# Performance work log

Hardware: AMD Instinct MI355X
Metric: run time of the kernel (lower is better)

The kernel has to match this reference:

```python
import jax, jax.numpy as jnp
import numpy as np

P_SIZES = (1, 2, 4)
O_SIZE = 32
EPS = 1e-5


def bilin_matrix(S, O):
    """Interpolation matrix (O, S) for torch UpsamplingBilinear2d (align_corners=True)."""
    if S == 1:
        return jnp.ones((O, 1), dtype=jnp.float32)
    pos = jnp.arange(O, dtype=jnp.float32) * ((S - 1) / (O - 1))
    lo = jnp.clip(jnp.floor(pos).astype(jnp.int32), 0, S - 2)
    frac = pos - lo.astype(jnp.float32)
    rows = jnp.arange(O)
    M = jnp.zeros((O, S), dtype=jnp.float32)
    M = M.at[rows, lo].add(1.0 - frac).at[rows, lo + 1].add(frac)
    return M


def setup_inputs() -> dict:
    key = jax.random.key(0)
    ks = jax.random.split(key, 12)
    n, C, H = 16, 512, 32
    c4 = C // 4      # 128, value/pyramid channels
    qk = c4 // 8     # 16, query/key channels inside SAE
    s = 0.05
    return {
        "x": jax.random.normal(ks[0], (n, C, H, H), jnp.float32),
        "rce_w": jax.random.normal(ks[1], (3, c4, C), jnp.float32) * s,   # 1x1 conv per pyramid scale
        "rce_b": jax.random.normal(ks[2], (3, c4), jnp.float32) * s,
        "q_w": jax.random.normal(ks[3], (qk, c4), jnp.float32) * s,       # SAE query 1x1 conv
        "q_b": jax.random.normal(ks[4], (qk,), jnp.float32) * s,
        "k_w": jax.random.normal(ks[5], (qk, c4), jnp.float32) * s,       # SAE key 1x1 conv
        "k_b": jax.random.normal(ks[6], (qk,), jnp.float32) * s,
        "value_w": jax.random.normal(ks[7], (c4, C), jnp.float32) * s,    # value 1x1 conv
        "value_b": jax.random.normal(ks[8], (c4,), jnp.float32) * s,
        "fusion_w": jax.random.normal(ks[9], (C, 3 * c4, 3, 3), jnp.float32) * s,  # 3x3 conv, no bias
        "bn_scale": 1.0 + jax.random.normal(ks[10], (C,), jnp.float32) * s,
        "bn_bias": jax.random.normal(ks[11], (C,), jnp.float32) * s,
        "gamma": jnp.asarray(0.5, jnp.float32),
    }


def reference(x, rce_w, rce_b, q_w, q_b, k_w, k_b, value_w, value_b,
              fusion_w, bn_scale, bn_bias, gamma):
    n, C, H, W = x.shape
    c4 = C // 4
    L = H * W

    # value projection: 1x1 conv then flatten -> (n, c4, L)
    proj_value = (jnp.einsum('oc,nchw->nohw', value_w, x)
                  + value_b[None, :, None, None]).reshape(n, c4, L)

    outs = []
    for i, sz in enumerate(P_SIZES):
        # AdaptiveAvgPool2d((sz, sz)) with divisible input -> exact uniform pooling
        pooled = x.reshape(n, C, sz, H // sz, sz, W // sz).mean(axis=(3, 5))
        # 1x1 conv C -> c4
        feat = jnp.einsum('oc,ncij->noij', rce_w[i], pooled) + rce_b[i][None, :, None, None]
        # bilinear upsample (align_corners=True) to (O_SIZE, O_SIZE)
        M = bilin_matrix(sz, O_SIZE)
        up = jnp.einsum('oi,pj,ncij->ncop', M, M, feat)  # (n, c4, H, W)
        # SAE: query/key 1x1 convs, flatten, bmm + softmax
        q = (jnp.einsum('oc,nchw->nohw', q_w, up) + q_b[None, :, None, None]).reshape(n, -1, L)
        k = (jnp.einsum('oc,nchw->nohw', k_w, up) + k_b[None, :, None, None]).reshape(n, -1, L)
        energy = jnp.einsum('ncl,ncm->nlm', q, k)        # (n, L, L)
        attn = jax.nn.softmax(energy, axis=-1)
        # temp = bmm(value, attn^T): temp[c,m] = sum_l value[c,l] * attn[m,l]
        outs.append(jnp.einsum('ncl,nml->ncm', proj_value, attn).reshape(n, c4, H, W))

    cat = jnp.concatenate(outs, axis=1)                  # (n, 3*c4, H, W)
    y = jax.lax.conv_general_dilated(
        cat, fusion_w, window_strides=(1, 1), padding=((1, 1), (1, 1)),
        dimension_numbers=('NCHW', 'OIHW', 'NCHW'))
    # BatchNorm2d in training mode (default): batch statistics over (N, H, W)
    mean = y.mean(axis=(0, 2, 3))
    var = y.var(axis=(0, 2, 3))
    y = (y - mean[None, :, None, None]) * (bn_scale / jnp.sqrt(var + EPS))[None, :, None, None] \
        + bn_bias[None, :, None, None]
    y = jax.nn.relu(y)
    return gamma * y + x
```

## Files before the change

kernel.cpp:

```cpp
#include <hip/hip_runtime.h>
#include <hip/hip_fp16.h>
#include <math.h>

#define OFF_COR   0u
#define OFF_PVH   2097152u
#define OFF_Y     3145728u
#define OFF_CATP  11534336u
#define OFF_QH    15085568u
#define OFF_KH    15347712u
#define OFF_POOL  16134144u
#define OFF_FEAT  16297984u
#define OFF_AW    16338944u
#define OFF_MEANS 17223680u
#define OFF_STAT  17225728u
#define OFF_VWH   17226752u

typedef __bf16 bf16x8 __attribute__((ext_vector_type(8)));
typedef _Float16 f16x8 __attribute__((ext_vector_type(8)));
typedef _Float16 f16x4 __attribute__((ext_vector_type(4)));
typedef float f32x4 __attribute__((ext_vector_type(4)));

__device__ __forceinline__ unsigned short f2bf(float f) {
  unsigned int u = __float_as_uint(f);
  unsigned int r = u + 0x7fff + ((u >> 16) & 1);
  return (unsigned short)(r >> 16);
}

__device__ __forceinline__ unsigned short f2h(float f) {
  union { _Float16 h; unsigned short u; } cv;
  cv.h = (_Float16)f;
  return cv.u;
}

__device__ __forceinline__ void gload_lds16(const void* g, void* l) {
  __builtin_amdgcn_global_load_lds(
      (const __attribute__((address_space(1))) unsigned int*)g,
      (__attribute__((address_space(3))) unsigned int*)l, 16, 0, 0);
}

__global__ __launch_bounds__(256) void pool_kernel(const float* __restrict__ x,
                                                   float* __restrict__ pool) {
  int b = blockIdx.x;
  int t = threadIdx.x;
  const float4* xp = (const float4*)(x + (size_t)b * 1024);
  float4 v = xp[t];
  float s4 = v.x + v.y + v.z + v.w;
  __shared__ float sm[256];
  __shared__ float p4s[16];
  sm[t] = s4;
  __syncthreads();
  if (t < 16) {
    int br = t >> 2, bc = t & 3;
    float s = 0.f;
#pragma unroll
    for (int rr = 0; rr < 8; ++rr) {
      int base = br * 64 + rr * 8 + bc * 2;
      s += sm[base] + sm[base + 1];
    }
    s *= (1.f / 64.f);
    p4s[t] = s;
    pool[(size_t)b * 20 + t] = s;
  }
  __syncthreads();
  if (t < 4) {
    int i2 = t >> 1, j2 = t & 1;
    float s = (p4s[(2*i2)*4 + 2*j2]     + p4s[(2*i2)*4 + 2*j2 + 1] +
               p4s[(2*i2+1)*4 + 2*j2]   + p4s[(2*i2+1)*4 + 2*j2 + 1]) * 0.25f;
    pool[(size_t)b * 20 + 16 + t] = s;
  }
}

__global__ __launch_bounds__(64) void feat_kernel(const float* __restrict__ pool,
                                                  const float* __restrict__ rce_w,
                                                  const float* __restrict__ rce_b,
                                                  float* __restrict__ feat) {
  int o = blockIdx.x, n = blockIdx.y, t = threadIdx.x;
  float part[20];
#pragma unroll
  for (int j = 0; j < 20; ++j) part[j] = 0.f;
  for (int c = t; c < 512; c += 64) {
    const float* pl = pool + ((size_t)n * 512 + c) * 20;
    float w2 = rce_w[(size_t)(128 + o) * 512 + c];
    float w4 = rce_w[(size_t)(256 + o) * 512 + c];
#pragma unroll
    for (int j = 0; j < 4; ++j)  part[j]     += w2 * pl[16 + j];
#pragma unroll
    for (int j = 0; j < 16; ++j) part[4 + j] += w4 * pl[j];
  }
  __shared__ float red[64][20];
#pragma unroll
  for (int j = 0; j < 20; ++j) red[t][j] = part[j];
  __syncthreads();
  if (t < 20) {
    float s = 0.f;
    for (int i = 0; i < 64; ++i) s += red[i][t];
    s += (t < 4) ? rce_b[128 + o] : rce_b[256 + o];
    feat[((size_t)n * 128 + o) * 20 + t] = s;
  }
}

__global__ __launch_bounds__(256) void qk2_kernel(const float* __restrict__ feat,
                                                  const float* __restrict__ q_w,
                                                  const float* __restrict__ q_b,
                                                  const float* __restrict__ k_w,
                                                  const float* __restrict__ k_b,
                                                  unsigned short* __restrict__ qh,
                                                  unsigned short* __restrict__ kh) {
  int n = blockIdx.x, t = threadIdx.x;
  __shared__ float fL[128 * 20];
  __shared__ float GH[2][16][20];
  for (int idx = t; idx < 2560; idx += 256) fL[idx] = feat[(size_t)n * 2560 + idx];
  __syncthreads();
  for (int idx = t; idx < 640; idx += 256) {
    int which = idx / 320, rem = idx % 320, qc = rem / 20, j = rem % 20;
    const float* w = which ? k_w : q_w;
    float s = which ? k_b[qc] : q_b[qc];
    for (int c = 0; c < 128; ++c) s += w[qc * 128 + c] * fL[c * 20 + j];
    GH[which][qc][j] = s;
  }
  __syncthreads();
  for (int it = 0; it < 16; ++it) {
    int row = t + 256 * it;
    int l = row & 1023, which = (row >> 10) & 1, s = row >> 11;
    int ry = l >> 5, cx = l & 31;
    int t0, t1, t2, t3;
    float w0, w1, w2, w3;
    if (s == 0) {
      float a = ry * (1.0f / 31.0f), b = cx * (1.0f / 31.0f);
      t0 = 0; t1 = 1; t2 = 2; t3 = 3;
      w0 = (1.f - a) * (1.f - b); w1 = (1.f - a) * b;
      w2 = a * (1.f - b);         w3 = a * b;
    } else {
      float pr = ry * (3.0f / 31.0f);
      int lr = (int)pr; if (lr > 2) lr = 2;
      float fr = pr - (float)lr;
      float pc = cx * (3.0f / 31.0f);
      int lc = (int)pc; if (lc > 2) lc = 2;
      float fc = pc - (float)lc;
      int base = 4 + lr * 4 + lc;
      t0 = base; t1 = base + 1; t2 = base + 4; t3 = base + 5;
      w0 = (1.f - fr) * (1.f - fc); w1 = (1.f - fr) * fc;
      w2 = fr * (1.f - fc);         w3 = fr * fc;
    }
    float val[16];
#pragma unroll
    for (int qc = 0; qc < 16; ++qc) {
      const float* G = GH[which][qc];
      val[qc] = w0 * G[t0] + w1 * G[t1] + w2 * G[t2] + w3 * G[t3];
    }
    unsigned short* dst = (which ? kh : qh) + (((size_t)(s * 16 + n) * 1024 + l) * 16);
#pragma unroll
    for (int u = 0; u < 4; ++u)
      *(ushort4*)(dst + 4 * u) = make_ushort4(f2h(val[4*u]), f2h(val[4*u+1]),
                                              f2h(val[4*u+2]), f2h(val[4*u+3]));
  }
}

__global__ __launch_bounds__(256) void xcast_kernel(const float* __restrict__ x,
                                                    unsigned short* __restrict__ xT) {
  int lt = blockIdx.x, ct = blockIdx.y, n = blockIdx.z;
  int l0 = lt * 64, c0 = ct * 64, t = threadIdx.x;
  __shared__ float tile[64 * 65];
#pragma unroll
  for (int i = 0; i < 16; ++i) {
    int idx = t + 256 * i;
    int c = idx >> 6, l = idx & 63;
    tile[c * 65 + l] = x[((size_t)n * 512 + c0 + c) * 1024 + l0 + l];
  }
  __syncthreads();
#pragma unroll
  for (int i = 0; i < 16; ++i) {
    int idx = t + 256 * i;
    int l = idx >> 6, c = idx & 63;
    xT[((size_t)n * 1024 + l0 + l) * 512 + c0 + c] = f2h(tile[c * 65 + l]);
  }
}

__global__ __launch_bounds__(256) void vwcast_kernel(const float* __restrict__ vw,
                                                     unsigned short* __restrict__ vwh) {
  int i = blockIdx.x * 256 + threadIdx.x;
  vwh[i] = f2h(vw[i]);
}

__global__ __launch_bounds__(256) void pvmm2_kernel(const unsigned short* __restrict__ vwh,
                                                    const unsigned short* __restrict__ xT,
                                                    const float* __restrict__ vb,
                                                    unsigned short* __restrict__ pvh) {
  int l0 = blockIdx.x * 64;
  int n = blockIdx.y;
  int t = threadIdx.x, lane = t & 63, wv = t >> 6;
  int wm = (wv & 1) * 64, wn = (wv >> 1) * 32;

  __shared__ short Asm[128 * 32];
  __shared__ short Bsm[64 * 32];

  int ar0 = t >> 2,        aq0 = (t & 3) ^ ((ar0 >> 1) & 3);
  int idx1 = t + 256; int ar1 = idx1 >> 2, aq1 = (idx1 & 3) ^ ((ar1 >> 1) & 3);
  int br  = t >> 2,        bq  = (t & 3) ^ ((br >> 1) & 3);
  const unsigned short* Ab0 = vwh + (size_t)ar0 * 512 + aq0 * 8;
  const unsigned short* Ab1 = vwh + (size_t)ar1 * 512 + aq1 * 8;
  const unsigned short* Bb  = xT + ((size_t)n * 1024 + l0 + br) * 512 + bq * 8;
  char* ldsA = (char*)Asm;
  char* ldsB = (char*)Bsm;
  int wvoff = wv * 1024;
  int r15 = lane & 15, kg = lane >> 4;
  int kq = kg ^ ((r15 >> 1) & 3);

  f32x4 acc[4][2];
#pragma unroll
  for (int i = 0; i < 4; ++i)
#pragma unroll
    for (int j = 0; j < 2; ++j) acc[i][j] = (f32x4){0.f, 0.f, 0.f, 0.f};

  for (int k0 = 0; k0 < 512; k0 += 32) {
    __syncthreads();
    gload_lds16(Ab0 + k0, ldsA + wvoff);
    gload_lds16(Ab1 + k0, ldsA + 4096 + wvoff);
    gload_lds16(Bb + k0,  ldsB + wvoff);
    __syncthreads();
    f16x8 af[4], bfr[2];
#pragma unroll
    for (int mt2 = 0; mt2 < 4; ++mt2)
      af[mt2] = *(const f16x8*)&Asm[(wm + mt2 * 16 + r15) * 32 + kq * 8];
#pragma unroll
    for (int nt2 = 0; nt2 < 2; ++nt2)
      bfr[nt2] = *(const f16x8*)&Bsm[(wn + nt2 * 16 + r15) * 32 + kq * 8];
#pragma unroll
    for (int mt2 = 0; mt2 < 4; ++mt2)
#pragma unroll
      for (int nt2 = 0; nt2 < 2; ++nt2)
        acc[mt2][nt2] = __builtin_amdgcn_mfma_f32_16x16x32_f16(af[mt2], bfr[nt2], acc[mt2][nt2], 0, 0, 0);
  }

  int c_lo = wm + (lane >> 4) * 4;
  int l_lo = wn + (lane & 15);
#pragma unroll
  for (int mt2 = 0; mt2 < 4; ++mt2)
#pragma unroll
    for (int nt2 = 0; nt2 < 2; ++nt2) {
      int l = l0 + l_lo + nt2 * 16;
#pragma unroll
      for (int r = 0; r < 4; ++r) {
        int c = c_lo + mt2 * 16 + r;
        pvh[((size_t)n * 128 + c) * 1024 + l] = f2h(acc[mt2][nt2][r] + vb[c]);
      }
    }
}

__global__ __launch_bounds__(256) void mean_kernel(const unsigned short* __restrict__ pvh,
                                                   float* __restrict__ means) {
  int c = blockIdx.x, n = blockIdx.y, t = threadIdx.x;
  f16x4 v = ((const f16x4*)(pvh + ((size_t)n * 128 + c) * 1024))[t];
  float s = (float)v[0] + (float)v[1] + (float)v[2] + (float)v[3];
  for (int o = 32; o > 0; o >>= 1) s += __shfl_down(s, o);
  __shared__ float wsum[4];
  if ((t & 63) == 0) wsum[t >> 6] = s;
  __syncthreads();
  if (t == 0) means[n * 128 + c] = (wsum[0] + wsum[1] + wsum[2] + wsum[3]) * (1.f / 1024.f);
}

__global__ __launch_bounds__(64) void basecor_kernel(const float* __restrict__ means,
                                                     const float* __restrict__ fw,
                                                     float* __restrict__ cor) {
  int oc = blockIdx.x, n = blockIdx.y, t = threadIdx.x;
  float S[9];
#pragma unroll
  for (int j = 0; j < 9; ++j) S[j] = 0.f;
  for (int c = t; c < 128; c += 64) {
    float m = means[n * 128 + c];
    const float* wp = fw + (size_t)oc * 3456 + c * 9;
#pragma unroll
    for (int j = 0; j < 9; ++j) S[j] += m * wp[j];
  }
  __shared__ float red[64][9];
  __shared__ float Sf[9];
#pragma unroll
  for (int j = 0; j < 9; ++j) red[t][j] = S[j];
  __syncthreads();
  if (t < 9) {
    float s = 0.f;
    for (int i = 0; i < 64; ++i) s += red[i][t];
    Sf[t] = s;
  }
  __syncthreads();
  if (t < 9) {
    int a = t / 3, b = t % 3;
    float s = 0.f;
#pragma unroll
    for (int ky = 0; ky < 3; ++ky) {
      if ((a == 0 && ky == 0) || (a == 2 && ky == 2)) continue;
#pragma unroll
      for (int kx = 0; kx < 3; ++kx) {
        if ((b == 0 && kx == 0) || (b == 2 && kx == 2)) continue;
        s += Sf[ky * 3 + kx];
      }
    }
    cor[((size_t)n * 512 + oc) * 9 + t] = s;
  }
}

__global__ __launch_bounds__(128) void fillcat_kernel(unsigned short* __restrict__ catp) {
  int b = blockIdx.x;
  int n = b / 132, e = b % 132;
  int py, px;
  if (e < 34)       { py = 0;          px = e; }
  else if (e < 68)  { py = 33;         px = e - 34; }
  else if (e < 100) { py = e - 68 + 1; px = 0; }
  else              { py = e - 100 + 1; px = 33; }
  unsigned int* row = (unsigned int*)(catp + ((size_t)n * 1156 + py * 34 + px) * 256);
  row[threadIdx.x] = 0u;
}

__global__ __launch_bounds__(256) void wcast_kernel(const float* __restrict__ fw,
                                                    unsigned short* __restrict__ Aw) {
  int oc = blockIdx.x, t = threadIdx.x;
  for (int j = t; j < 2304; j += 256) {
    int seg = j >> 8, ic2 = j & 255;
    Aw[(size_t)oc * 2304 + j] = f2bf(fw[(size_t)oc * 3456 + (128 + ic2) * 9 + seg]);
  }
}

__global__ __launch_bounds__(256) void fattn_kernel(const unsigned short* __restrict__ qh,
                                                    const unsigned short* __restrict__ kh,
                                                    const unsigned short* __restrict__ pvh,
                                                    unsigned short* __restrict__ catp) {
  int m0 = blockIdx.x * 64;
  int n = blockIdx.y, sc = blockIdx.z;
  int t = threadIdx.x, lane = t & 63, wv = t >> 6;
  int wc = (wv >> 1) * 64;
  int wm2 = (wv & 1) * 32;
  int r15 = lane & 15, kg = lane >> 4;
  int kq = kg ^ ((r15 >> 1) & 3);

  const unsigned short* qb  = qh + ((size_t)(sc * 16 + n) * 1024 + m0 + wv * 16) * 16;
  const unsigned short* kb  = kh + ((size_t)(sc * 16 + n) * 1024) * 16;
  const unsigned short* pvb = pvh + (size_t)n * 128 * 1024;

  __shared__ short PVs[2 * 128 * 32];
  __shared__ _Float16 Us[64 * 72];
  __shared__ float rsum[64];

  f16x8 zf = {0, 0, 0, 0, 0, 0, 0, 0};
  f16x8 qa = (kg < 2) ? *(const f16x8*)(qb + r15 * 16 + kg * 8) : zf;

  int prow = t >> 2;
  int aq = (t & 3) ^ ((prow >> 1) & 3);
  const unsigned short* Pb0 = pvb + (size_t)prow * 1024 + aq * 8;
  const unsigned short* Pb1 = pvb + (size_t)(prow + 64) * 1024 + aq * 8;
  char* ldsPV = (char*)PVs;
  int wvoff = wv * 1024;

  f32x4 acc[4][2];
#pragma unroll
  for (int i = 0; i < 4; ++i)
#pragma unroll
    for (int j = 0; j < 2; ++j) acc[i][j] = (f32x4){0.f, 0.f, 0.f, 0.f};
  float rs[4] = {0.f, 0.f, 0.f, 0.f};

  for (int it = 0; it < 16; ++it) {
    int l0 = it * 64;
    __syncthreads();
    gload_lds16(Pb0 + l0,      ldsPV + wvoff);
    gload_lds16(Pb1 + l0,      ldsPV + 4096 + wvoff);
    gload_lds16(Pb0 + l0 + 32, ldsPV + 8192 + wvoff);
    gload_lds16(Pb1 + l0 + 32, ldsPV + 12288 + wvoff);

    f32x4 sacc[4];
#pragma unroll
    for (int lt = 0; lt < 4; ++lt) {
      f16x8 kbf = (kg < 2)
        ? *(const f16x8*)(kb + (size_t)(l0 + lt * 16 + r15) * 16 + kg * 8) : zf;
      sacc[lt] = __builtin_amdgcn_mfma_f32_16x16x32_f16(qa, kbf, (f32x4){0.f,0.f,0.f,0.f}, 0, 0, 0);
    }
#pragma unroll
    for (int lt = 0; lt < 4; ++lt)
#pragma unroll
      for (int r = 0; r < 4; ++r) {
        float e = __expf(sacc[lt][r]);
        Us[(wv * 16 + kg * 4 + r) * 72 + lt * 16 + r15] = (_Float16)e;
        rs[r] += e;
      }
    __syncthreads();

#pragma unroll
    for (int ks = 0; ks < 2; ++ks) {
      f16x8 bfr[2];
#pragma unroll
      for (int nt = 0; nt < 2; ++nt)
        bfr[nt] = *(const f16x8*)&Us[(wm2 + nt * 16 + r15) * 72 + ks * 32 + kg * 8];
#pragma unroll
      for (int ct = 0; ct < 4; ++ct) {
        f16x8 af = *(const f16x8*)&PVs[ks * 4096 + (wc + ct * 16 + r15) * 32 + kq * 8];
#pragma unroll
        for (int nt = 0; nt < 2; ++nt)
          acc[ct][nt] = __builtin_amdgcn_mfma_f32_16x16x32_f16(af, bfr[nt], acc[ct][nt], 0, 0, 0);
      }
    }
  }

#pragma unroll
  for (int r = 0; r < 4; ++r) {
    rs[r] += __shfl_xor(rs[r], 1);
    rs[r] += __shfl_xor(rs[r], 2);
    rs[r] += __shfl_xor(rs[r], 4);
    rs[r] += __shfl_xor(rs[r], 8);
  }
  if (r15 == 0) {
#pragma unroll
    for (int r = 0; r < 4; ++r) rsum[wv * 16 + kg * 4 + r] = rs[r];
  }
  __syncthreads();

#pragma unroll
  for (int nt = 0; nt < 2; ++nt) {
    float inv = 1.f / rsum[wm2 + nt * 16 + r15];
    int pix = m0 + wm2 + nt * 16 + r15;
    unsigned short* ob = catp + ((size_t)n * 1156 + ((pix >> 5) + 1) * 34 + (pix & 31) + 1) * 256
                       + sc * 128 + wc + kg * 4;
#pragma unroll
    for (int ct = 0; ct < 4; ++ct) {
      ushort4 o = make_ushort4(f2bf(acc[ct][nt][0] * inv), f2bf(acc[ct][nt][1] * inv),
                               f2bf(acc[ct][nt][2] * inv), f2bf(acc[ct][nt][3] * inv));
      *(ushort4*)(ob + ct * 16) = o;
    }
  }
}

__device__ __forceinline__ void conv_stage(const unsigned short* __restrict__ Aw,
                                           const unsigned short* __restrict__ catp,
                                           size_t abase0, size_t abase1,
                                           size_t bbase0, size_t bbase1,
                                           int s, char* la, char* lb, int wvoff) {
  int seg = s >> 2;
  size_t akk  = (size_t)s * 64;
  size_t boff = (size_t)((seg / 3) * 34 + (seg % 3)) * 256 + (size_t)(s & 3) * 64;
  gload_lds16(Aw + abase0 + akk,          la + wvoff);
  gload_lds16(Aw + abase1 + akk,          la + 4096 + wvoff);
  gload_lds16(Aw + abase0 + akk + 32,     la + 8192 + wvoff);
  gload_lds16(Aw + abase1 + akk + 32,     la + 12288 + wvoff);
  gload_lds16(catp + bbase0 + boff,       lb + wvoff);
  gload_lds16(catp + bbase1 + boff,       lb + 4096 + wvoff);
  gload_lds16(catp + bbase0 + boff + 32,  lb + 8192 + wvoff);
  gload_lds16(catp + bbase1 + boff + 32,  lb + 12288 + wvoff);
}

__device__ __forceinline__ void conv_comp(const short* As_, const short* Bs_,
                                          int wm, int wn, int r15, int kq,
                                          f32x4 acc[4][4]) {
  bf16x8 af[4], bf[4];
#pragma unroll
  for (int mt = 0; mt < 4; ++mt)
    af[mt] = *(const bf16x8*)&As_[(wm + mt * 16 + r15) * 32 + kq * 8];
#pragma unroll
  for (int nt = 0; nt < 4; ++nt)
    bf[nt] = *(const bf16x8*)&Bs_[(wn + nt * 16 + r15) * 32 + kq * 8];
#pragma unroll
  for (int mt = 0; mt < 4; ++mt)
#pragma unroll
    for (int nt = 0; nt < 4; ++nt)
      acc[mt][nt] = __builtin_amdgcn_mfma_f32_16x16x32_bf16(af[mt], bf[nt], acc[mt][nt], 0, 0, 0);
}

__global__ __launch_bounds__(256) void convmm_kernel(const unsigned short* __restrict__ Aw,
                                                     const unsigned short* __restrict__ catp,
                                                     const float* __restrict__ cor,
                                                     float* __restrict__ y) {
  int ntile = blockIdx.x;
  int n = ntile >> 3, y0 = (ntile & 7) * 4;
  int m0 = blockIdx.y * 128;
  int t = threadIdx.x;
  int lane = t & 63, wv = t >> 6;
  int wm = (wv & 1) * 64, wn = (wv >> 1) * 64;

  __shared__ short Asm[2 * 2 * 128 * 32];
  __shared__ short Bsm[2 * 2 * 128 * 32];

  int idx0 = t, idx1 = t + 256;
  int ar0 = idx0 >> 2, aq0 = (idx0 & 3) ^ ((ar0 >> 1) & 3);
  int ar1 = idx1 >> 2, aq1 = (idx1 & 3) ^ ((ar1 >> 1) & 3);
  size_t abase0 = (size_t)(m0 + ar0) * 2304 + aq0 * 8;
  size_t abase1 = (size_t)(m0 + ar1) * 2304 + aq1 * 8;
  size_t bbase0 = ((size_t)n * 1156 + (size_t)(y0 + (ar0 >> 5)) * 34 + (ar0 & 31)) * 256 + aq0 * 8;
  size_t bbase1 = ((size_t)n * 1156 + (size_t)(y0 + (ar1 >> 5)) * 34 + (ar1 & 31)) * 256 + aq1 * 8;
  char* ldsA = (char*)Asm;
  char* ldsB = (char*)Bsm;
  int wvoff = wv * 1024;

  int r15 = lane & 15, kg = lane >> 4;
  int kq = kg ^ ((r15 >> 1) & 3);

  f32x4 acc[4][4];
#pragma unroll
  for (int i = 0; i < 4; ++i)
#pragma unroll
    for (int j = 0; j < 4; ++j) acc[i][j] = (f32x4){0.f, 0.f, 0.f, 0.f};

  conv_stage(Aw, catp, abase0, abase1, bbase0, bbase1, 0, ldsA, ldsB, wvoff);
  __syncthreads();

#pragma unroll 2
  for (int s = 0; s < 36; ++s) {
    char* la = ldsA + (s & 1) * 16384;
    char* lb = ldsB + (s & 1) * 16384;
    if (s < 35)
      conv_stage(Aw, catp, abase0, abase1, bbase0, bbase1, s + 1,
                 ldsA + ((s + 1) & 1) * 16384, ldsB + ((s + 1) & 1) * 16384, wvoff);
    conv_comp((const short*)la,          (const short*)lb,          wm, wn, r15, kq, acc);
    conv_comp((const short*)(la + 8192), (const short*)(lb + 8192), wm, wn, r15, kq, acc);
    __syncthreads();
  }

  int pixbase = (ntile & 7) * 128 + wn + (lane & 15);
  int ocbase = m0 + wm + (lane >> 4) * 4;
#pragma unroll
  for (int mt = 0; mt < 4; ++mt)
#pragma unroll
    for (int nt = 0; nt < 4; ++nt) {
      int oc = ocbase + mt * 16;
      int pix = pixbase + nt * 16;
      int py = pix >> 5, px = pix & 31;
      int yc = (py == 0) ? 0 : ((py == 31) ? 2 : 1);
      int xc = (px == 0) ? 0 : ((px == 31) ? 2 : 1);
      const float* cp = cor + ((size_t)n * 512 + oc) * 9 + yc * 3 + xc;
      float* yp = y + ((size_t)n * 512 + oc) * 1024 + pix;
#pragma unroll
      for (int r = 0; r < 4; ++r) yp[(size_t)r * 1024] = acc[mt][nt][r] + cp[(size_t)r * 9];
    }
}

__global__ __launch_bounds__(256) void bnstat_kernel(const float* __restrict__ y,
                                                     const float* __restrict__ bn_scale,
                                                     const float* __restrict__ bn_bias,
                                                     float* __restrict__ stats) {
  int oc = blockIdx.x, t = threadIdx.x;
  float s = 0.f, ss = 0.f;
  for (int n = 0; n < 16; ++n) {
    float4 v = ((const float4*)(y + ((size_t)n * 512 + oc) * 1024))[t];
    s  += v.x + v.y + v.z + v.w;
    ss += v.x * v.x + v.y * v.y + v.z * v.z + v.w * v.w;
  }
  for (int o = 32; o > 0; o >>= 1) {
    s  += __shfl_down(s, o);
    ss += __shfl_down(ss, o);
  }
  __shared__ float rs[4], rss[4];
  if ((t & 63) == 0) { rs[t >> 6] = s; rss[t >> 6] = ss; }
  __syncthreads();
  if (t == 0) {
    float S = rs[0] + rs[1] + rs[2] + rs[3];
    float SS = rss[0] + rss[1] + rss[2] + rss[3];
    float mean = S * (1.f / 16384.f);
    float var = SS * (1.f / 16384.f) - mean * mean;
    float se = bn_scale[oc] / sqrtf(var + 1e-5f);
    stats[oc * 2] = se;
    stats[oc * 2 + 1] = bn_bias[oc] - mean * se;
  }
}

__global__ __launch_bounds__(256) void final_kernel(const float* __restrict__ y,
                                                    const float* __restrict__ x,
                                                    const float* __restrict__ stats,
                                                    const float* __restrict__ gamma,
                                                    float* __restrict__ outp) {
  int b = blockIdx.x;
  int c = b & 511;
  int t = threadIdx.x;
  float se = stats[c * 2], sh = stats[c * 2 + 1], g = gamma[0];
  float4 yv = ((const float4*)(y + (size_t)b * 1024))[t];
  float4 xv = ((const float4*)(x + (size_t)b * 1024))[t];
  float4 o;
  o.x = g * fmaxf(yv.x * se + sh, 0.f) + xv.x;
  o.y = g * fmaxf(yv.y * se + sh, 0.f) + xv.y;
  o.z = g * fmaxf(yv.z * se + sh, 0.f) + xv.z;
  o.w = g * fmaxf(yv.w * se + sh, 0.f) + xv.w;
  ((float4*)(outp + (size_t)b * 1024))[t] = o;
}

extern "C" void kernel_launch(void* const* d_in, const int* in_sizes, int n_in,
                              void* d_out, int out_size, void* d_ws, size_t ws_size,
                              hipStream_t stream) {
  const float* x        = (const float*)d_in[0];
  const float* rce_w    = (const float*)d_in[1];
  const float* rce_b    = (const float*)d_in[2];
  const float* q_w      = (const float*)d_in[3];
  const float* q_b      = (const float*)d_in[4];
  const float* k_w      = (const float*)d_in[5];
  const float* k_b      = (const float*)d_in[6];
  const float* value_w  = (const float*)d_in[7];
  const float* value_b  = (const float*)d_in[8];
  const float* fw       = (const float*)d_in[9];
  const float* bn_scale = (const float*)d_in[10];
  const float* bn_bias  = (const float*)d_in[11];
  const float* gamma    = (const float*)d_in[12];

  float* ws    = (float*)d_ws;
  float* cor   = ws + OFF_COR;
  unsigned short* pvh = (unsigned short*)(ws + OFF_PVH);
  float* ybuf  = ws + OFF_Y;
  unsigned short* xTbuf = (unsigned short*)(ws + OFF_Y);
  unsigned short* catp = (unsigned short*)(ws + OFF_CATP);
  unsigned short* qh   = (unsigned short*)(ws + OFF_QH);
  unsigned short* kh   = (unsigned short*)(ws + OFF_KH);
  float* pool  = ws + OFF_POOL;
  float* feat  = ws + OFF_FEAT;
  unsigned short* Aw = (unsigned short*)(ws + OFF_AW);
  float* means = ws + OFF_MEANS;
  float* stats = ws + OFF_STAT;
  unsigned short* vwh = (unsigned short*)(ws + OFF_VWH);
  float* outp  = (float*)d_out;

  hipLaunchKernelGGL(pool_kernel,    dim3(8192),       dim3(256), 0, stream, x, pool);
  hipLaunchKernelGGL(feat_kernel,    dim3(128, 16),    dim3(64),  0, stream, pool, rce_w, rce_b, feat);
  hipLaunchKernelGGL(qk2_kernel,     dim3(16),         dim3(256), 0, stream, feat, q_w, q_b, k_w, k_b, qh, kh);
  hipLaunchKernelGGL(xcast_kernel,   dim3(16, 8, 16),  dim3(256), 0, stream, x, xTbuf);
  hipLaunchKernelGGL(vwcast_kernel,  dim3(256),        dim3(256), 0, stream, value_w, vwh);
  hipLaunchKernelGGL(pvmm2_kernel,   dim3(16, 16),     dim3(256), 0, stream, vwh, xTbuf, value_b, pvh);
  hipLaunchKernelGGL(mean_kernel,    dim3(128, 16),    dim3(256), 0, stream, pvh, means);
  hipLaunchKernelGGL(basecor_kernel, dim3(512, 16),    dim3(64),  0, stream, means, fw, cor);
  hipLaunchKernelGGL(fillcat_kernel, dim3(2112),       dim3(128), 0, stream, catp);
  hipLaunchKernelGGL(wcast_kernel,   dim3(512),        dim3(256), 0, stream, fw, Aw);
  hipLaunchKernelGGL(fattn_kernel,   dim3(16, 16, 2),  dim3(256), 0, stream, qh, kh, pvh, catp);
  hipLaunchKernelGGL(convmm_kernel,  dim3(128, 4),     dim3(256), 0, stream, Aw, catp, cor, ybuf);
  hipLaunchKernelGGL(bnstat_kernel,  dim3(512),        dim3(256), 0, stream, ybuf, bn_scale, bn_bias, stats);
  hipLaunchKernelGGL(final_kernel,   dim3(8192),       dim3(256), 0, stream, ybuf, x, stats, gamma, outp);
}
```

Before: 259.7 us.

## Double-buffer PV tiles in attention kernel and split qk2 across more blocks

The fused attention kernel now keeps two LDS buffers for the projected-value tiles. It prefetches the next tile while the current one is consumed, and replaces the __syncthreads calls with explicit waitcnt and s_barrier so the global-to-LDS load overlaps the QK/exp and PV MFMA work. Separately, qk2_kernel is launched on a 16x8 grid, with each block handling 2 of the 16 row iterations instead of all of them, which raises parallelism for that small kernel. The cost is double the LDS for the PV buffers, which may lower occupancy, plus a redundant recompute of the per-batch G matrix in every y-block.

```diff
diff --git a/kernel.cpp b/kernel.cpp
--- a/kernel.cpp
+++ b/kernel.cpp
@@ -119,7 +119,7 @@
     GH[which][qc][j] = s;
   }
   __syncthreads();
-  for (int it = 0; it < 16; ++it) {
+  for (int it = blockIdx.y * 2; it < blockIdx.y * 2 + 2; ++it) {
     int row = t + 256 * it;
     int l = row & 1023, which = (row >> 10) & 1, s = row >> 11;
     int ry = l >> 5, cx = l & 31;
@@ -336,7 +336,7 @@
   const unsigned short* kb  = kh + ((size_t)(sc * 16 + n) * 1024) * 16;
   const unsigned short* pvb = pvh + (size_t)n * 128 * 1024;
 
-  __shared__ short PVs[2 * 128 * 32];
+  __shared__ short PVs[2 * 2 * 128 * 32];
   __shared__ _Float16 Us[64 * 72];
   __shared__ float rsum[64];
 
@@ -357,21 +357,30 @@
     for (int j = 0; j < 2; ++j) acc[i][j] = (f32x4){0.f, 0.f, 0.f, 0.f};
   float rs[4] = {0.f, 0.f, 0.f, 0.f};
 
+  gload_lds16(Pb0,      ldsPV + wvoff);
+  gload_lds16(Pb1,      ldsPV + 4096 + wvoff);
+  gload_lds16(Pb0 + 32, ldsPV + 8192 + wvoff);
+  gload_lds16(Pb1 + 32, ldsPV + 12288 + wvoff);
+
   for (int it = 0; it < 16; ++it) {
+    int cur = it & 1;
     int l0 = it * 64;
-    __syncthreads();
-    gload_lds16(Pb0 + l0,      ldsPV + wvoff);
-    gload_lds16(Pb1 + l0,      ldsPV + 4096 + wvoff);
-    gload_lds16(Pb0 + l0 + 32, ldsPV + 8192 + wvoff);
-    gload_lds16(Pb1 + l0 + 32, ldsPV + 12288 + wvoff);
-
+    f16x8 kbf[4];
+#pragma unroll
+    for (int lt = 0; lt < 4; ++lt)
+      kbf[lt] = (kg < 2)
+        ? *(const f16x8*)(kb + (size_t)(l0 + lt * 16 + r15) * 16 + kg * 8) : zf;
+    if (it < 15) {
+      char* dst = ldsPV + (cur ^ 1) * 16384 + wvoff;
+      gload_lds16(Pb0 + l0 + 64, dst);
+      gload_lds16(Pb1 + l0 + 64, dst + 4096);
+      gload_lds16(Pb0 + l0 + 96, dst + 8192);
+      gload_lds16(Pb1 + l0 + 96, dst + 12288);
+    }
     f32x4 sacc[4];
 #pragma unroll
-    for (int lt = 0; lt < 4; ++lt) {
-      f16x8 kbf = (kg < 2)
-        ? *(const f16x8*)(kb + (size_t)(l0 + lt * 16 + r15) * 16 + kg * 8) : zf;
-      sacc[lt] = __builtin_amdgcn_mfma_f32_16x16x32_f16(qa, kbf, (f32x4){0.f,0.f,0.f,0.f}, 0, 0, 0);
-    }
+    for (int lt = 0; lt < 4; ++lt)
+      sacc[lt] = __builtin_amdgcn_mfma_f32_16x16x32_f16(qa, kbf[lt], (f32x4){0.f,0.f,0.f,0.f}, 0, 0, 0);
 #pragma unroll
     for (int lt = 0; lt < 4; ++lt)
 #pragma unroll
@@ -380,8 +389,9 @@
         Us[(wv * 16 + kg * 4 + r) * 72 + lt * 16 + r15] = (_Float16)e;
         rs[r] += e;
       }
-    __syncthreads();
-
+    asm volatile("s_waitcnt vmcnt(4) lgkmcnt(0)" ::: "memory");
+    __builtin_amdgcn_s_barrier();
+    __builtin_amdgcn_sched_barrier(0);
 #pragma unroll
     for (int ks = 0; ks < 2; ++ks) {
       f16x8 bfr[2];
@@ -390,12 +400,15 @@
         bfr[nt] = *(const f16x8*)&Us[(wm2 + nt * 16 + r15) * 72 + ks * 32 + kg * 8];
 #pragma unroll
       for (int ct = 0; ct < 4; ++ct) {
-        f16x8 af = *(const f16x8*)&PVs[ks * 4096 + (wc + ct * 16 + r15) * 32 + kq * 8];
+        f16x8 af = *(const f16x8*)&PVs[cur * 8192 + ks * 4096 + (wc + ct * 16 + r15) * 32 + kq * 8];
 #pragma unroll
         for (int nt = 0; nt < 2; ++nt)
           acc[ct][nt] = __builtin_amdgcn_mfma_f32_16x16x32_f16(af, bfr[nt], acc[ct][nt], 0, 0, 0);
       }
     }
+    asm volatile("s_waitcnt lgkmcnt(0)" ::: "memory");
+    __builtin_amdgcn_s_barrier();
+    __builtin_amdgcn_sched_barrier(0);
   }
 
 #pragma unroll
@@ -611,7 +624,7 @@
 
   hipLaunchKernelGGL(pool_kernel,    dim3(8192),       dim3(256), 0, stream, x, pool);
   hipLaunchKernelGGL(feat_kernel,    dim3(128, 16),    dim3(64),  0, stream, pool, rce_w, rce_b, feat);
-  hipLaunchKernelGGL(qk2_kernel,     dim3(16),         dim3(256), 0, stream, feat, q_w, q_b, k_w, k_b, qh, kh);
+  hipLaunchKernelGGL(qk2_kernel,     dim3(16, 8),      dim3(256), 0, stream, feat, q_w, q_b, k_w, k_b, qh, kh);
   hipLaunchKernelGGL(xcast_kernel,   dim3(16, 8, 16),  dim3(256), 0, stream, x, xTbuf);
   hipLaunchKernelGGL(vwcast_kernel,  dim3(256),        dim3(256), 0, stream, value_w, vwh);
   hipLaunchKernelGGL(pvmm2_kernel,   dim3(16, 16),     dim3(256), 0, stream, vwh, xTbuf, value_b, pvh);
```

Measured after the change: 244.6 us. 1.06x faster.
